# Performance work log

Hardware: AMD Instinct MI355X
Metric: run time of the kernel (lower is better)

The kernel has to match this reference:

```python
import jax, jax.numpy as jnp
import numpy as np

K = 32  # manager.k
EPS = 1e-12  # F.normalize eps


def _l2norm(x, axis):
    n = jnp.linalg.norm(x, axis=axis, keepdims=True)
    return x / jnp.maximum(n, EPS)


def setup_inputs() -> dict:
    key = jax.random.key(0)
    k0, k1, k2, k3, k4, k5 = jax.random.split(key, 6)
    B, H, S, D = 16, 50, 256, 256
    return {
        "news_selection_embedding": jax.random.normal(k0, (B, H, S, D), jnp.float32),
        "news_embedding": jax.random.normal(k1, (B, H, S, D), jnp.float32),
        "user_repr": jax.random.normal(k2, (B, 1, D), jnp.float32),
        "news_repr": jax.random.normal(k3, (B, H, D), jnp.float32),
        "his_attn_mask": jnp.ones((B, H, S), jnp.float32),
        "his_refined_mask": jax.random.randint(k4, (B, H, S), 0, 2, jnp.int32),
        "segment_embedding": jax.random.normal(k5, (H, 1, D), jnp.float32) * 0.02,
    }


def reference(news_selection_embedding, news_embedding, user_repr, news_repr,
              his_attn_mask, his_refined_mask, segment_embedding):
    B, H, S, D = news_embedding.shape
    # drop the leading [CLS]-like token
    sel = news_selection_embedding[:, :, 1:]   # [B,H,S-1,D]
    txt = news_embedding[:, :, 1:]             # [B,H,S-1,D]
    am = his_attn_mask[:, :, 1:]               # [B,H,S-1]

    # diversify=False: selection query is the user representation, normalized over D
    q_n = _l2norm(user_repr[:, 0, :], axis=-1)         # [B,D]
    sel_n = _l2norm(sel, axis=-1)                      # [B,H,S-1,D]
    scores = jnp.einsum('bhsd,bd->bhs', sel_n, q_n)    # cosine scores [B,H,S-1]

    # keep first K positions always selectable
    keep_k = jnp.zeros((S - 1,), jnp.float32).at[:K].set(1.0)
    valid = (his_refined_mask[:, :, 1:].astype(jnp.float32) + keep_k) != 0
    scores = jnp.where(valid, scores, -jnp.inf)

    score_k, kid = jax.lax.top_k(scores, K)            # sorted descending, [B,H,K]

    ps_terms = jnp.take_along_axis(txt, kid[..., None], axis=2)  # [B,H,K,D]
    ps_term_mask = jnp.take_along_axis(am, kid, axis=2)          # [B,H,K]

    w = jax.nn.softmax(score_k, axis=-1)               # [B,H,K]
    ps_terms = ps_terms * w[..., None] + segment_embedding  # segment_embedding [H,1,D]

    # flatten=True, sep_his=False
    ps_terms = ps_terms.reshape(B, H * K, D)
    ps_term_mask = ps_term_mask.reshape(B, H * K)
    return ps_terms, ps_term_mask, kid
```

## Files before the change

### kernel.cpp

```cpp
#include <hip/hip_runtime.h>
#include <math.h>

#define KSEL 32
#define DDIM 256
#define SDIM 256
#define SM1  255
#define EPSN 1e-12f

__global__ __launch_bounds__(256) void matching_reducer_kernel(
    const float* __restrict__ nse,
    const float* __restrict__ ne,
    const float* __restrict__ ur,
    const float* __restrict__ am,
    const int*   __restrict__ rm,
    const float* __restrict__ seg,
    float* __restrict__ out_terms,
    float* __restrict__ out_mask,
    float* __restrict__ out_kid,
    int H)
{
    const int bh   = blockIdx.x;
    const int b    = bh / H;
    const int h    = bh % H;
    const int tid  = threadIdx.x;
    const int lane = tid & 63;
    const int wave = tid >> 6;
    const int g    = tid >> 4;
    const int t    = tid & 15;

    __shared__ float  s_dot[256][17];
    __shared__ float  s_ss[256][17];
    __shared__ float  s_scores[256];
    __shared__ int    s_rows[256];
    __shared__ unsigned long long s_key[256];
    __shared__ int    s_wbase[4];
    __shared__ int    s_nv;
    __shared__ int    s_kid[KSEL];
    __shared__ float  s_w[KSEL];
    __shared__ float4 s_seg[64];

    if (tid < 64) {
        s_seg[tid] = reinterpret_cast<const float4*>(seg + (size_t)h * DDIM)[tid];
    }
    s_scores[tid] = -INFINITY;

    const int* rmb = rm + (size_t)bh * SDIM + 1;
    const bool valid = (tid < SM1) && ((rmb[tid] != 0) || (tid < KSEL));
    const unsigned long long ball = __ballot(valid);
    if (lane == 0) s_wbase[wave] = __popcll(ball);

    const float4* qv = reinterpret_cast<const float4*>(ur + (size_t)b * DDIM);
    float4 qf[4];
    #pragma unroll
    for (int j = 0; j < 4; ++j) qf[j] = qv[t + 16 * j];
    float qq = 0.f;
    #pragma unroll
    for (int j = 0; j < 4; ++j)
        qq += qf[j].x * qf[j].x + qf[j].y * qf[j].y + qf[j].z * qf[j].z + qf[j].w * qf[j].w;
    #pragma unroll
    for (int o = 8; o > 0; o >>= 1) qq += __shfl_xor(qq, o, 16);
    const float inv_q = 1.0f / fmaxf(sqrtf(qq), EPSN);

    __syncthreads();
    if (tid == 0) {
        int acc = 0;
        #pragma unroll
        for (int w2 = 0; w2 < 4; ++w2) { int c = s_wbase[w2]; s_wbase[w2] = acc; acc += c; }
        s_nv = acc;
    }
    __syncthreads();
    if (valid) {
        const int off = __popcll(ball & ((1ull << lane) - 1ull));
        s_rows[s_wbase[wave] + off] = tid;
    }
    __syncthreads();

    const int nv = s_nv;
    const float* selb = nse + ((size_t)bh * SDIM + 1) * DDIM;
    for (int i = g; i < nv; i += 32) {
        const int  rowA = s_rows[i];
        const bool hasB = (i + 16) < nv;
        const int  rowB = hasB ? s_rows[i + 16] : rowA;
        const float4* xa = reinterpret_cast<const float4*>(selb + (size_t)rowA * DDIM);
        const float4* xb = reinterpret_cast<const float4*>(selb + (size_t)rowB * DDIM);
        float4 va[4], vb[4];
        #pragma unroll
        for (int j = 0; j < 4; ++j) { va[j] = xa[t + 16 * j]; vb[j] = xb[t + 16 * j]; }
        float dotA = 0.f, ssA = 0.f, dotB = 0.f, ssB = 0.f;
        #pragma unroll
        for (int j = 0; j < 4; ++j) {
            dotA += va[j].x * qf[j].x + va[j].y * qf[j].y + va[j].z * qf[j].z + va[j].w * qf[j].w;
            ssA  += va[j].x * va[j].x + va[j].y * va[j].y + va[j].z * va[j].z + va[j].w * va[j].w;
            dotB += vb[j].x * qf[j].x + vb[j].y * qf[j].y + vb[j].z * qf[j].z + vb[j].w * qf[j].w;
            ssB  += vb[j].x * vb[j].x + vb[j].y * vb[j].y + vb[j].z * vb[j].z + vb[j].w * vb[j].w;
        }
        s_dot[rowA][t] = dotA;
        s_ss [rowA][t] = ssA;
        if (hasB) { s_dot[rowB][t] = dotB; s_ss[rowB][t] = ssB; }
    }
    __syncthreads();

    if (valid) {
        float dv = 0.f, sv = 0.f;
        #pragma unroll
        for (int j = 0; j < 16; ++j) { dv += s_dot[tid][j]; sv += s_ss[tid][j]; }
        s_scores[tid] = dv * inv_q / fmaxf(sqrtf(sv), EPSN);
    }
    __syncthreads();

    unsigned long long v;
    {
        const float s = s_scores[tid];
        unsigned u = __float_as_uint(s);
        unsigned f = (u & 0x80000000u) ? ~u : (u | 0x80000000u);
        unsigned kd = ~f;
        v = ((unsigned long long)kd << 32) | (unsigned)tid;
    }
    #pragma unroll
    for (unsigned k = 2; k <= 256; k <<= 1) {
        #pragma unroll
        for (unsigned j = k >> 1; j > 0; j >>= 1) {
            unsigned long long p;
            if (j >= 64) {
                s_key[tid] = v;
                __syncthreads();
                p = s_key[tid ^ j];
                __syncthreads();
            } else {
                p = __shfl_xor(v, (int)j, 64);
            }
            const bool up      = ((tid & k) == 0);
            const bool upper   = (tid & j) != 0;
            const bool takeMax = (up == upper);
            v = takeMax ? (v > p ? v : p) : (v < p ? v : p);
        }
    }

    if (tid < KSEL) {
        const int idx = (int)(v & 0xFFFFFFFFu);
        s_kid[tid] = idx;
        out_kid [(size_t)bh * KSEL + tid] = (float)idx;
        out_mask[(size_t)bh * KSEL + tid] = am[(size_t)bh * SDIM + 1 + idx];
        const float sc = s_scores[idx];
        const float m  = __shfl(sc, 0, 64);
        const float e  = expf(sc - m);
        float sum = e;
        #pragma unroll
        for (int o = 16; o > 0; o >>= 1) sum += __shfl_xor(sum, o, 32);
        s_w[tid] = e / sum;
    }
    __syncthreads();

    const float* txtb = ne + ((size_t)bh * SDIM + 1) * DDIM;
    float* outb = out_terms + (size_t)bh * KSEL * DDIM;
    const int d4 = tid & 63;
    #pragma unroll
    for (int p = 0; p < 8; ++p) {
        const int k    = p * 4 + (tid >> 6);
        const int kidx = s_kid[k];
        const float wk = s_w[k];
        float4 x  = reinterpret_cast<const float4*>(txtb + (size_t)kidx * DDIM)[d4];
        float4 sg = s_seg[d4];
        float4 r;
        r.x = x.x * wk + sg.x;
        r.y = x.y * wk + sg.y;
        r.z = x.z * wk + sg.z;
        r.w = x.w * wk + sg.w;
        reinterpret_cast<float4*>(outb + (size_t)k * DDIM)[d4] = r;
    }
}

extern "C" void kernel_launch(void* const* d_in, const int* in_sizes, int n_in,
                              void* d_out, int out_size, void* d_ws, size_t ws_size,
                              hipStream_t stream) {
    const float* nse = (const float*)d_in[0];
    const float* ne  = (const float*)d_in[1];
    const float* ur  = (const float*)d_in[2];
    const float* am  = (const float*)d_in[4];
    const int*   rm  = (const int*)  d_in[5];
    const float* seg = (const float*)d_in[6];

    const int B = in_sizes[2] / DDIM;
    const int H = in_sizes[6] / DDIM;

    float* out = (float*)d_out;
    const size_t n_terms = (size_t)B * H * KSEL * DDIM;
    const size_t n_mask  = (size_t)B * H * KSEL;

    matching_reducer_kernel<<<dim3(B * H), dim3(256), 0, stream>>>(
        nse, ne, ur, am, rm, seg,
        out, out + n_terms, out + n_terms + n_mask, H);
}
```

Measured before the change: 33.14 us.

## Prefetch always-valid rows before compaction and unroll score loop to four rows

Loads for the first 32 selection rows, which are always valid because of the keep-first-K rule, are issued at kernel start. Their dot products are computed while the validity ballot and prefix compaction run, hiding that setup behind memory latency. The remaining rows are processed four per thread group per iteration instead of two, increasing loads in flight. This raises register pressure and may reduce occupancy.

```diff
diff --git a/kernel.cpp b/kernel.cpp
--- a/kernel.cpp
+++ b/kernel.cpp
@@ -39,6 +39,18 @@
     __shared__ float  s_w[KSEL];
     __shared__ float4 s_seg[64];
 
+    const float* selb = nse + ((size_t)bh * SDIM + 1) * DDIM;
+    const float4* xa0 = reinterpret_cast<const float4*>(selb + (size_t)g * DDIM);
+    const float4* xb0 = reinterpret_cast<const float4*>(selb + (size_t)(g + 16) * DDIM);
+    float4 vA[4], vB[4];
+    #pragma unroll
+    for (int j = 0; j < 4; ++j) { vA[j] = xa0[t + 16 * j]; vB[j] = xb0[t + 16 * j]; }
+
+    const float4* qv = reinterpret_cast<const float4*>(ur + (size_t)b * DDIM);
+    float4 qf[4];
+    #pragma unroll
+    for (int j = 0; j < 4; ++j) qf[j] = qv[t + 16 * j];
+
     if (tid < 64) {
         s_seg[tid] = reinterpret_cast<const float4*>(seg + (size_t)h * DDIM)[tid];
     }
@@ -49,10 +61,6 @@
     const unsigned long long ball = __ballot(valid);
     if (lane == 0) s_wbase[wave] = __popcll(ball);
 
-    const float4* qv = reinterpret_cast<const float4*>(ur + (size_t)b * DDIM);
-    float4 qf[4];
-    #pragma unroll
-    for (int j = 0; j < 4; ++j) qf[j] = qv[t + 16 * j];
     float qq = 0.f;
     #pragma unroll
     for (int j = 0; j < 4; ++j)
@@ -73,30 +81,61 @@
         const int off = __popcll(ball & ((1ull << lane) - 1ull));
         s_rows[s_wbase[wave] + off] = tid;
     }
+
+    {
+        float dotA = 0.f, ssA = 0.f, dotB = 0.f, ssB = 0.f;
+        #pragma unroll
+        for (int j = 0; j < 4; ++j) {
+            dotA += vA[j].x * qf[j].x + vA[j].y * qf[j].y + vA[j].z * qf[j].z + vA[j].w * qf[j].w;
+            ssA  += vA[j].x * vA[j].x + vA[j].y * vA[j].y + vA[j].z * vA[j].z + vA[j].w * vA[j].w;
+            dotB += vB[j].x * qf[j].x + vB[j].y * qf[j].y + vB[j].z * qf[j].z + vB[j].w * qf[j].w;
+            ssB  += vB[j].x * vB[j].x + vB[j].y * vB[j].y + vB[j].z * vB[j].z + vB[j].w * vB[j].w;
+        }
+        s_dot[g][t]      = dotA;
+        s_ss [g][t]      = ssA;
+        s_dot[g + 16][t] = dotB;
+        s_ss [g + 16][t] = ssB;
+    }
     __syncthreads();
 
     const int nv = s_nv;
-    const float* selb = nse + ((size_t)bh * SDIM + 1) * DDIM;
-    for (int i = g; i < nv; i += 32) {
-        const int  rowA = s_rows[i];
-        const bool hasB = (i + 16) < nv;
-        const int  rowB = hasB ? s_rows[i + 16] : rowA;
-        const float4* xa = reinterpret_cast<const float4*>(selb + (size_t)rowA * DDIM);
-        const float4* xb = reinterpret_cast<const float4*>(selb + (size_t)rowB * DDIM);
-        float4 va[4], vb[4];
-        #pragma unroll
-        for (int j = 0; j < 4; ++j) { va[j] = xa[t + 16 * j]; vb[j] = xb[t + 16 * j]; }
-        float dotA = 0.f, ssA = 0.f, dotB = 0.f, ssB = 0.f;
+    for (int i = 32 + g; i < nv; i += 64) {
+        const bool h1 = (i + 16) < nv;
+        const bool h2 = (i + 32) < nv;
+        const bool h3 = (i + 48) < nv;
+        const int r0 = s_rows[i];
+        const int r1 = h1 ? s_rows[i + 16] : r0;
+        const int r2 = h2 ? s_rows[i + 32] : r0;
+        const int r3 = h3 ? s_rows[i + 48] : r0;
+        const float4* x0 = reinterpret_cast<const float4*>(selb + (size_t)r0 * DDIM);
+        const float4* x1 = reinterpret_cast<const float4*>(selb + (size_t)r1 * DDIM);
+        const float4* x2 = reinterpret_cast<const float4*>(selb + (size_t)r2 * DDIM);
+        const float4* x3 = reinterpret_cast<const float4*>(selb + (size_t)r3 * DDIM);
+        float4 v0[4], v1[4], v2[4], v3[4];
         #pragma unroll
         for (int j = 0; j < 4; ++j) {
-            dotA += va[j].x * qf[j].x + va[j].y * qf[j].y + va[j].z * qf[j].z + va[j].w * qf[j].w;
-            ssA  += va[j].x * va[j].x + va[j].y * va[j].y + va[j].z * va[j].z + va[j].w * va[j].w;
-            dotB += vb[j].x * qf[j].x + vb[j].y * qf[j].y + vb[j].z * qf[j].z + vb[j].w * qf[j].w;
-            ssB  += vb[j].x * vb[j].x + vb[j].y * vb[j].y + vb[j].z * vb[j].z + vb[j].w * vb[j].w;
-        }
-        s_dot[rowA][t] = dotA;
-        s_ss [rowA][t] = ssA;
-        if (hasB) { s_dot[rowB][t] = dotB; s_ss[rowB][t] = ssB; }
+            v0[j] = x0[t + 16 * j];
+            v1[j] = x1[t + 16 * j];
+            v2[j] = x2[t + 16 * j];
+            v3[j] = x3[t + 16 * j];
+        }
+        float d0 = 0.f, s0 = 0.f, d1 = 0.f, s1 = 0.f;
+        float d2 = 0.f, s2 = 0.f, d3 = 0.f, s3 = 0.f;
+        #pragma unroll
+        for (int j = 0; j < 4; ++j) {
+            d0 += v0[j].x * qf[j].x + v0[j].y * qf[j].y + v0[j].z * qf[j].z + v0[j].w * qf[j].w;
+            s0 += v0[j].x * v0[j].x + v0[j].y * v0[j].y + v0[j].z * v0[j].z + v0[j].w * v0[j].w;
+            d1 += v1[j].x * qf[j].x + v1[j].y * qf[j].y + v1[j].z * qf[j].z + v1[j].w * qf[j].w;
+            s1 += v1[j].x * v1[j].x + v1[j].y * v1[j].y + v1[j].z * v1[j].z + v1[j].w * v1[j].w;
+            d2 += v2[j].x * qf[j].x + v2[j].y * qf[j].y + v2[j].z * qf[j].z + v2[j].w * qf[j].w;
+            s2 += v2[j].x * v2[j].x + v2[j].y * v2[j].y + v2[j].z * v2[j].z + v2[j].w * v2[j].w;
+            d3 += v3[j].x * qf[j].x + v3[j].y * qf[j].y + v3[j].z * qf[j].z + v3[j].w * qf[j].w;
+            s3 += v3[j].x * v3[j].x + v3[j].y * v3[j].y + v3[j].z * v3[j].z + v3[j].w * v3[j].w;
+        }
+        s_dot[r0][t] = d0; s_ss[r0][t] = s0;
+        if (h1) { s_dot[r1][t] = d1; s_ss[r1][t] = s1; }
+        if (h2) { s_dot[r2][t] = d2; s_ss[r2][t] = s2; }
+        if (h3) { s_dot[r3][t] = d3; s_ss[r3][t] = s3; }
     }
     __syncthreads();
 
```

Result: no change. 32.68 us (-1.4%).
